# Optimization experiments

Measured on AMD Instinct MI355X. Metric: run time of the kernel, lower is better.

The kernel has to match this reference:

```python
import jax, jax.numpy as jnp
import numpy as np

EXP_CLAMP = 1.0e6
DENOM_EPS = 1e-10
LRELU_ALPHA = 0.01


def setup_inputs() -> dict:
    key = jax.random.key(0)
    k1, k2, k3, k4, k5, k6 = jax.random.split(key, 6)
    B, N, E, F = 4, 16384, 262144, 64
    h = jax.random.normal(k1, (B, N, F), dtype=jnp.float32)
    edge = jax.random.randint(k2, (B, E, 2), 0, N, dtype=jnp.int32)
    edge_num = jax.random.randint(k3, (B,), 1, E, dtype=jnp.int32)
    edge_weight = jax.random.uniform(k4, (B, E), dtype=jnp.float32)
    W = jax.random.normal(k5, (F, F), dtype=jnp.float32) * 0.15  # xavier-ish scale
    a = jax.random.normal(k6, (1, 2 * F), dtype=jnp.float32) * 0.12
    return {"h": h, "edge": edge, "edge_num": edge_num,
            "edge_weight": edge_weight, "W": W, "a": a}


def _seg_sum(src, idx, num_segments):
    # src: [E, ...], idx: [E] -> [num_segments, ...]
    return jax.ops.segment_sum(src, idx, num_segments=num_segments)


def reference(h, edge, edge_num, edge_weight, W, a):
    B, N, Fin = h.shape
    E = edge.shape[1]
    # linear transform: Wh = h @ W^T  -> [B, N, Fout]
    Wh = jnp.einsum('bnf,of->bno', h, W)
    ctr = edge[:, :, 0]  # [B, E]
    nbr = edge[:, :, 1]  # [B, E]
    Wh_c = jnp.take_along_axis(Wh, ctr[:, :, None], axis=1)  # [B, E, Fout]
    Wh_n = jnp.take_along_axis(Wh, nbr[:, :, None], axis=1)  # [B, E, Fout]
    a_input = jnp.concatenate([Wh_c, Wh_n], axis=-1) * edge_weight[:, :, None]
    # attention logits: leakyrelu(a_input @ a^T), squeeze to [B, E]
    att1 = jax.nn.leaky_relu(jnp.einsum('bek,k->be', a_input, a[0]), LRELU_ALPHA)
    # per-batch valid-edge mask (edges beyond edge_num zeroed, as in torch loop)
    mask = (jnp.arange(E, dtype=jnp.int32)[None, :] < edge_num[:, None])
    x_exp = jnp.clip(jnp.exp(att1), 0.0, EXP_CLAMP) * mask.astype(att1.dtype)
    # segment softmax denominator over center nodes
    denom = DENOM_EPS + jax.vmap(_seg_sum, in_axes=(0, 0, None))(x_exp, ctr, N)  # [B, N]
    att = x_exp / jnp.take_along_axis(denom, ctr, axis=1)  # [B, E]
    # weighted neighbor aggregation via scatter-add on center index
    att_Wh = Wh_n * att[:, :, None]  # masked edges already have att == 0
    h_prime = jax.vmap(_seg_sum, in_axes=(0, 0, None))(att_Wh, ctr, N)  # [B, N, Fout]
    return jax.nn.relu(h_prime)
```

## Files before the change

### kernel.cpp

```cpp
#include <hip/hip_runtime.h>

#define BB 4
#define NN 16384
#define EE 262144
#define FF 64
#define ROWS (BB * NN)
#define CAP 64
#define CHUNKS 64
#define CHUNK_E (EE / CHUNKS)
#define TILE_R 256
#define HALF_R (NN / 2)

typedef __bf16 bf16x8 __attribute__((ext_vector_type(8)));
typedef float  f32x4  __attribute__((ext_vector_type(4)));

__device__ __forceinline__ unsigned short f32_to_bf16(float f) {
    unsigned int u = __float_as_uint(f);
    u += 0x7FFFu + ((u >> 16) & 1u);
    return (unsigned short)(u >> 16);
}

__global__ __launch_bounds__(256) void mfma_kernel(
    const float* __restrict__ h, const float* __restrict__ W,
    const float* __restrict__ a,
    unsigned short* __restrict__ Wh,
    float* __restrict__ sc, float* __restrict__ sn)
{
    __shared__ float wc[FF], wn[FF];
    const int t = threadIdx.x;
    const int lane = t & 63;
    const int m = lane & 15;
    const int q = lane >> 4;

    if (t < 128) {
        const int f = t & 63;
        const float* av = a + (t >> 6) * FF;
        float s = 0.0f;
        #pragma unroll 8
        for (int o = 0; o < FF; ++o)
            s = fmaf(av[o], W[o * FF + f], s);
        (t < 64 ? wc : wn)[f] = s;
    }

    bf16x8 bfrag[4][2];
    #pragma unroll
    for (int nt = 0; nt < 4; ++nt) {
        const float* wr = W + (nt * 16 + m) * FF;
        #pragma unroll
        for (int kh = 0; kh < 2; ++kh) {
            const float4 v0 = *(const float4*)(wr + kh * 32 + q * 8);
            const float4 v1 = *(const float4*)(wr + kh * 32 + q * 8 + 4);
            bf16x8 b;
            b[0] = (__bf16)v0.x; b[1] = (__bf16)v0.y;
            b[2] = (__bf16)v0.z; b[3] = (__bf16)v0.w;
            b[4] = (__bf16)v1.x; b[5] = (__bf16)v1.y;
            b[6] = (__bf16)v1.z; b[7] = (__bf16)v1.w;
            bfrag[nt][kh] = b;
        }
    }

    __syncthreads();

    const int waveId = (blockIdx.x * 256 + t) >> 6;
    const int R0 = waveId * 16;
    const float* hr = h + (size_t)(R0 + m) * FF;
    bf16x8 af[2];
    float s1 = 0.0f, s2 = 0.0f;
    #pragma unroll
    for (int kh = 0; kh < 2; ++kh) {
        const float4 v0 = *(const float4*)(hr + kh * 32 + q * 8);
        const float4 v1 = *(const float4*)(hr + kh * 32 + q * 8 + 4);
        bf16x8 aa;
        aa[0] = (__bf16)v0.x; aa[1] = (__bf16)v0.y;
        aa[2] = (__bf16)v0.z; aa[3] = (__bf16)v0.w;
        aa[4] = (__bf16)v1.x; aa[5] = (__bf16)v1.y;
        aa[6] = (__bf16)v1.z; aa[7] = (__bf16)v1.w;
        af[kh] = aa;
        const int fb = kh * 32 + q * 8;
        const float4 c0 = *(const float4*)&wc[fb];
        const float4 c1 = *(const float4*)&wc[fb + 4];
        const float4 n0 = *(const float4*)&wn[fb];
        const float4 n1 = *(const float4*)&wn[fb + 4];
        s1 = fmaf(v0.x, c0.x, fmaf(v0.y, c0.y, fmaf(v0.z, c0.z, fmaf(v0.w, c0.w, s1))));
        s1 = fmaf(v1.x, c1.x, fmaf(v1.y, c1.y, fmaf(v1.z, c1.z, fmaf(v1.w, c1.w, s1))));
        s2 = fmaf(v0.x, n0.x, fmaf(v0.y, n0.y, fmaf(v0.z, n0.z, fmaf(v0.w, n0.w, s2))));
        s2 = fmaf(v1.x, n1.x, fmaf(v1.y, n1.y, fmaf(v1.z, n1.z, fmaf(v1.w, n1.w, s2))));
    }
    s1 += __shfl_xor(s1, 16); s2 += __shfl_xor(s2, 16);
    s1 += __shfl_xor(s1, 32); s2 += __shfl_xor(s2, 32);
    if (lane < 16) { sc[R0 + m] = s1; sn[R0 + m] = s2; }

    #pragma unroll
    for (int nt = 0; nt < 4; ++nt) {
        f32x4 acc = {0.f, 0.f, 0.f, 0.f};
        acc = __builtin_amdgcn_mfma_f32_16x16x32_bf16(af[0], bfrag[nt][0], acc, 0, 0, 0);
        acc = __builtin_amdgcn_mfma_f32_16x16x32_bf16(af[1], bfrag[nt][1], acc, 0, 0, 0);
        #pragma unroll
        for (int i = 0; i < 4; ++i)
            Wh[(size_t)(R0 + q * 4 + i) * FF + nt * 16 + m] = f32_to_bf16(acc[i]);
    }
}

__global__ __launch_bounds__(1024) void hist_kernel(
    const int* __restrict__ edge, const int* __restrict__ edge_num,
    unsigned short* __restrict__ histG)
{
    __shared__ unsigned int hist[HALF_R];
    const int g = blockIdx.x;
    const int half = g & 1;
    const int c = (g >> 1) & (CHUNKS - 1);
    const int b = g >> 7;
    const int t = threadIdx.x;
    const int en = edge_num[b];
    const int e0 = c * CHUNK_E;
    if (e0 >= en) return;

    for (int r = t; r < HALF_R; r += 1024) hist[r] = 0u;
    __syncthreads();

    const int2* ep = (const int2*)edge + (size_t)b * EE + e0;
    const int nAct = min(en - e0, CHUNK_E);
    for (int j = t; j < nAct; j += 1024) {
        const int2 e2 = ep[j];
        if ((e2.x >> 13) == half)
            atomicAdd(&hist[e2.x & (HALF_R - 1)], 1u);
    }
    __syncthreads();

    ushort2* out2 = (ushort2*)(histG + (size_t)(b * CHUNKS + c) * NN + half * HALF_R);
    for (int r2 = t; r2 < HALF_R / 2; r2 += 1024) {
        ushort2 v;
        v.x = (unsigned short)hist[2 * r2];
        v.y = (unsigned short)hist[2 * r2 + 1];
        out2[r2] = v;
    }
}

__global__ __launch_bounds__(256) void scan_kernel(
    const int* __restrict__ edge_num,
    unsigned short* __restrict__ histG, int* __restrict__ cnt)
{
    __shared__ unsigned short tile[CHUNKS][TILE_R];
    const int g = blockIdx.x;
    const int b = g >> 6, tl = g & 63;
    const int r0 = tl * TILE_R;
    const int t = threadIdx.x;
    const int en = edge_num[b];
    const int nact = min((en + CHUNK_E - 1) / CHUNK_E, CHUNKS);

    for (int c = 0; c < nact; ++c)
        tile[c][t] = histG[(size_t)(b * CHUNKS + c) * NN + r0 + t];
    __syncthreads();

    unsigned int acc = 0;
    for (int c = 0; c < nact; ++c) {
        const unsigned int v = tile[c][t];
        tile[c][t] = (unsigned short)(acc > 65535u ? 65535u : acc);
        acc += v;
    }
    cnt[b * NN + r0 + t] = (int)acc;

    for (int c = 0; c < nact; ++c)
        histG[(size_t)(b * CHUNKS + c) * NN + r0 + t] = tile[c][t];
}

__global__ __launch_bounds__(1024) void scatter_kernel(
    const int* __restrict__ edge, const int* __restrict__ edge_num,
    const unsigned short* __restrict__ baseG,
    const float* __restrict__ sc, const float* __restrict__ sn,
    const float* __restrict__ ew,
    unsigned int* __restrict__ payload)
{
    __shared__ unsigned int slotA[HALF_R];
    __shared__ float scL[HALF_R];
    const int g = blockIdx.x;
    const int half = g & 1;
    const int c = (g >> 1) & (CHUNKS - 1);
    const int b = g >> 7;
    const int t = threadIdx.x;
    const int en = edge_num[b];
    const int e0 = c * CHUNK_E;
    if (e0 >= en) return;

    const int rbase = half * HALF_R;
    const ushort2* b2 = (const ushort2*)(baseG + (size_t)(b * CHUNKS + c) * NN + rbase);
    for (int r2 = t; r2 < HALF_R / 2; r2 += 1024) {
        const ushort2 v = b2[r2];
        slotA[2 * r2]     = v.x;
        slotA[2 * r2 + 1] = v.y;
    }
    const float* scH = sc + b * NN + rbase;
    for (int r = t; r < HALF_R; r += 1024)
        scL[r] = scH[r];
    __syncthreads();

    const int2* ep = (const int2*)edge + (size_t)b * EE + e0;
    const int nAct = min(en - e0, CHUNK_E);
    const float* snB = sn + b * NN;
    const float* ewB = ew + (size_t)b * EE + e0;
    unsigned int* payB = payload + (size_t)b * NN * CAP;

    for (int j = t; j < nAct; j += 1024) {
        const int2 e2 = ep[j];
        if ((e2.x >> 13) != half) continue;
        const int rl = e2.x & (HALF_R - 1);
        const float wgt = ewB[j];
        const float s0 = wgt * (scL[rl] + snB[e2.y]);
        const float s1 = s0 > 0.0f ? s0 : 0.01f * s0;
        const float xe = fminf(__expf(s1), 1000000.0f);
        const unsigned int slot = atomicAdd(&slotA[rl], 1u);
        if (slot < CAP)
            payB[(size_t)e2.x * CAP + slot] =
                ((__float_as_uint(xe) + 0x2000u) & 0xFFFFC000u) | (unsigned int)e2.y;
    }
}

__global__ __launch_bounds__(256) void gather_kernel(
    const int* __restrict__ cnt, const unsigned int* __restrict__ payload,
    const uint2* __restrict__ Wh2,
    float* __restrict__ out)
{
    const int bi = blockIdx.x;
    const int xcd = bi & 7;
    const int batch = xcd >> 1;
    const int within = ((bi >> 3) << 1) | (xcd & 1);
    const int w = threadIdx.x >> 6;
    const int lane = threadIdx.x & 63;
    const int r = lane >> 4;
    const int f = lane & 15;
    const int gbase = lane & 48;
    const int rq = within * 4 + w;
    const int row = batch * NN + rq * 4 + r;

    const unsigned int* pl = payload + (size_t)row * CAP;
    const uint2* WhB = Wh2 + (size_t)batch * NN * 16;

    int deg = cnt[row];
    unsigned int raw = pl[f];
    if (deg > CAP) deg = CAP;

    int jmax = deg;
    jmax = max(jmax, __shfl_xor(jmax, 16));
    jmax = max(jmax, __shfl_xor(jmax, 32));

    float a0 = 0.f, a1 = 0.f, a2 = 0.f, a3 = 0.f, pdsum = 0.f;

    for (int base = 0; base < jmax; base += 16) {
        const unsigned int p = (base + f < deg) ? raw : 0u;
        pdsum += __uint_as_float(p & 0xFFFFC000u);

        unsigned int rawN = 0u;
        if (base + 16 < jmax) rawN = pl[base + 16 + f];

        const int lim = min(16, jmax - base);
        for (int j4 = 0; j4 < lim; j4 += 4) {
            const unsigned int pv0 = __shfl(p, gbase + j4 + 0);
            const unsigned int pv1 = __shfl(p, gbase + j4 + 1);
            const unsigned int pv2 = __shfl(p, gbase + j4 + 2);
            const unsigned int pv3 = __shfl(p, gbase + j4 + 3);
            const uint2 w0 = WhB[(size_t)(pv0 & 0x3FFFu) * 16 + f];
            const uint2 w1 = WhB[(size_t)(pv1 & 0x3FFFu) * 16 + f];
            const uint2 w2 = WhB[(size_t)(pv2 & 0x3FFFu) * 16 + f];
            const uint2 w3 = WhB[(size_t)(pv3 & 0x3FFFu) * 16 + f];
            const float xe0 = __uint_as_float(pv0 & 0xFFFFC000u);
            const float xe1 = __uint_as_float(pv1 & 0xFFFFC000u);
            const float xe2 = __uint_as_float(pv2 & 0xFFFFC000u);
            const float xe3 = __uint_as_float(pv3 & 0xFFFFC000u);
            a0 = fmaf(xe0, __uint_as_float(w0.x << 16),         a0);
            a1 = fmaf(xe0, __uint_as_float(w0.x & 0xFFFF0000u), a1);
            a2 = fmaf(xe0, __uint_as_float(w0.y << 16),         a2);
            a3 = fmaf(xe0, __uint_as_float(w0.y & 0xFFFF0000u), a3);
            a0 = fmaf(xe1, __uint_as_float(w1.x << 16),         a0);
            a1 = fmaf(xe1, __uint_as_float(w1.x & 0xFFFF0000u), a1);
            a2 = fmaf(xe1, __uint_as_float(w1.y << 16),         a2);
            a3 = fmaf(xe1, __uint_as_float(w1.y & 0xFFFF0000u), a3);
            a0 = fmaf(xe2, __uint_as_float(w2.x << 16),         a0);
            a1 = fmaf(xe2, __uint_as_float(w2.x & 0xFFFF0000u), a1);
            a2 = fmaf(xe2, __uint_as_float(w2.y << 16),         a2);
            a3 = fmaf(xe2, __uint_as_float(w2.y & 0xFFFF0000u), a3);
            a0 = fmaf(xe3, __uint_as_float(w3.x << 16),         a0);
            a1 = fmaf(xe3, __uint_as_float(w3.x & 0xFFFF0000u), a1);
            a2 = fmaf(xe3, __uint_as_float(w3.y << 16),         a2);
            a3 = fmaf(xe3, __uint_as_float(w3.y & 0xFFFF0000u), a3);
        }
        raw = rawN;
    }

    pdsum += __shfl_xor(pdsum, 1);
    pdsum += __shfl_xor(pdsum, 2);
    pdsum += __shfl_xor(pdsum, 4);
    pdsum += __shfl_xor(pdsum, 8);

    const float inv = 1.0f / (1e-10f + pdsum);
    float4 o;
    o.x = fmaxf(a0 * inv, 0.0f);
    o.y = fmaxf(a1 * inv, 0.0f);
    o.z = fmaxf(a2 * inv, 0.0f);
    o.w = fmaxf(a3 * inv, 0.0f);
    ((float4*)out)[(size_t)row * 16 + f] = o;
}

extern "C" void kernel_launch(void* const* d_in, const int* in_sizes, int n_in,
                              void* d_out, int out_size, void* d_ws, size_t ws_size,
                              hipStream_t stream)
{
    const float* h        = (const float*)d_in[0];
    const int*   edge     = (const int*)  d_in[1];
    const int*   edge_num = (const int*)  d_in[2];
    const float* ew       = (const float*)d_in[3];
    const float* W        = (const float*)d_in[4];
    const float* a        = (const float*)d_in[5];
    float* out = (float*)d_out;

    unsigned short* Wh = (unsigned short*)d_ws;
    float* sc        = (float*)(Wh + (size_t)BB * NN * FF);
    float* sn        = sc + ROWS;
    int*   cnt       = (int*)(sn + ROWS);
    unsigned int* payload = (unsigned int*)(cnt + ROWS);
    unsigned short* histG = (unsigned short*)(payload + (size_t)ROWS * CAP);

    mfma_kernel<<<1024, 256, 0, stream>>>(h, W, a, Wh, sc, sn);

    hist_kernel<<<BB * CHUNKS * 2, 1024, 0, stream>>>(edge, edge_num, histG);

    scan_kernel<<<BB * (NN / TILE_R), 256, 0, stream>>>(edge_num, histG, cnt);

    scatter_kernel<<<BB * CHUNKS * 2, 1024, 0, stream>>>(edge, edge_num, histG,
                                                         sc, sn, ew, payload);

    gather_kernel<<<4096, 256, 0, stream>>>(cnt, payload,
                                            (const uint2*)Wh, out);
}
```

Baseline: 130.3 us.

## Fuse the node-transform MFMA kernel with the edge histogram kernel

```diff
diff --git a/kernel.cpp b/kernel.cpp
--- a/kernel.cpp
+++ b/kernel.cpp
@@ -10,6 +10,7 @@
 #define CHUNK_E (EE / CHUNKS)
 #define TILE_R 256
 #define HALF_R (NN / 2)
+#define QUART_R (NN / 4)
 
 typedef __bf16 bf16x8 __attribute__((ext_vector_type(8)));
 typedef float  f32x4  __attribute__((ext_vector_type(4)));
@@ -20,17 +21,28 @@
     return (unsigned short)(u >> 16);
 }
 
-__global__ __launch_bounds__(256) void mfma_kernel(
+__global__ __launch_bounds__(256) void mfma_hist_kernel(
     const float* __restrict__ h, const float* __restrict__ W,
     const float* __restrict__ a,
+    const int* __restrict__ edge, const int* __restrict__ edge_num,
     unsigned short* __restrict__ Wh,
-    float* __restrict__ sc, float* __restrict__ sn)
+    float* __restrict__ sc, float* __restrict__ sn,
+    unsigned short* __restrict__ histG)
 {
     __shared__ float wc[FF], wn[FF];
+    __shared__ unsigned int hist[QUART_R];
     const int t = threadIdx.x;
     const int lane = t & 63;
     const int m = lane & 15;
     const int q = lane >> 4;
+
+    const int g = blockIdx.x;
+    const int b = g >> 8;
+    const int c = (g >> 2) & (CHUNKS - 1);
+    const int quarter = g & 3;
+    const int en = edge_num[b];
+    const int e0 = c * CHUNK_E;
+    const bool active = (e0 < en);
 
     if (t < 128) {
         const int f = t & 63;
@@ -41,6 +53,7 @@
             s = fmaf(av[o], W[o * FF + f], s);
         (t < 64 ? wc : wn)[f] = s;
     }
+    for (int r = t; r < QUART_R; r += 256) hist[r] = 0u;
 
     bf16x8 bfrag[4][2];
     #pragma unroll
@@ -50,89 +63,75 @@
         for (int kh = 0; kh < 2; ++kh) {
             const float4 v0 = *(const float4*)(wr + kh * 32 + q * 8);
             const float4 v1 = *(const float4*)(wr + kh * 32 + q * 8 + 4);
-            bf16x8 b;
-            b[0] = (__bf16)v0.x; b[1] = (__bf16)v0.y;
-            b[2] = (__bf16)v0.z; b[3] = (__bf16)v0.w;
-            b[4] = (__bf16)v1.x; b[5] = (__bf16)v1.y;
-            b[6] = (__bf16)v1.z; b[7] = (__bf16)v1.w;
-            bfrag[nt][kh] = b;
+            bf16x8 bb;
+            bb[0] = (__bf16)v0.x; bb[1] = (__bf16)v0.y;
+            bb[2] = (__bf16)v0.z; bb[3] = (__bf16)v0.w;
+            bb[4] = (__bf16)v1.x; bb[5] = (__bf16)v1.y;
+            bb[6] = (__bf16)v1.z; bb[7] = (__bf16)v1.w;
+            bfrag[nt][kh] = bb;
         }
     }
 
     __syncthreads();
 
-    const int waveId = (blockIdx.x * 256 + t) >> 6;
-    const int R0 = waveId * 16;
-    const float* hr = h + (size_t)(R0 + m) * FF;
-    bf16x8 af[2];
-    float s1 = 0.0f, s2 = 0.0f;
-    #pragma unroll
-    for (int kh = 0; kh < 2; ++kh) {
-        const float4 v0 = *(const float4*)(hr + kh * 32 + q * 8);
-        const float4 v1 = *(const float4*)(hr + kh * 32 + q * 8 + 4);
-        bf16x8 aa;
-        aa[0] = (__bf16)v0.x; aa[1] = (__bf16)v0.y;
-        aa[2] = (__bf16)v0.z; aa[3] = (__bf16)v0.w;
-        aa[4] = (__bf16)v1.x; aa[5] = (__bf16)v1.y;
-        aa[6] = (__bf16)v1.z; aa[7] = (__bf16)v1.w;
-        af[kh] = aa;
-        const int fb = kh * 32 + q * 8;
-        const float4 c0 = *(const float4*)&wc[fb];
-        const float4 c1 = *(const float4*)&wc[fb + 4];
-        const float4 n0 = *(const float4*)&wn[fb];
-        const float4 n1 = *(const float4*)&wn[fb + 4];
-        s1 = fmaf(v0.x, c0.x, fmaf(v0.y, c0.y, fmaf(v0.z, c0.z, fmaf(v0.w, c0.w, s1))));
-        s1 = fmaf(v1.x, c1.x, fmaf(v1.y, c1.y, fmaf(v1.z, c1.z, fmaf(v1.w, c1.w, s1))));
-        s2 = fmaf(v0.x, n0.x, fmaf(v0.y, n0.y, fmaf(v0.z, n0.z, fmaf(v0.w, n0.w, s2))));
-        s2 = fmaf(v1.x, n1.x, fmaf(v1.y, n1.y, fmaf(v1.z, n1.z, fmaf(v1.w, n1.w, s2))));
-    }
-    s1 += __shfl_xor(s1, 16); s2 += __shfl_xor(s2, 16);
-    s1 += __shfl_xor(s1, 32); s2 += __shfl_xor(s2, 32);
-    if (lane < 16) { sc[R0 + m] = s1; sn[R0 + m] = s2; }
-
-    #pragma unroll
-    for (int nt = 0; nt < 4; ++nt) {
-        f32x4 acc = {0.f, 0.f, 0.f, 0.f};
-        acc = __builtin_amdgcn_mfma_f32_16x16x32_bf16(af[0], bfrag[nt][0], acc, 0, 0, 0);
-        acc = __builtin_amdgcn_mfma_f32_16x16x32_bf16(af[1], bfrag[nt][1], acc, 0, 0, 0);
+    {
+        const int waveId = g * 4 + (t >> 6);
+        const int R0 = waveId * 16;
+        const float* hr = h + (size_t)(R0 + m) * FF;
+        bf16x8 af[2];
+        float s1 = 0.0f, s2 = 0.0f;
         #pragma unroll
-        for (int i = 0; i < 4; ++i)
-            Wh[(size_t)(R0 + q * 4 + i) * FF + nt * 16 + m] = f32_to_bf16(acc[i]);
-    }
-}
-
-__global__ __launch_bounds__(1024) void hist_kernel(
-    const int* __restrict__ edge, const int* __restrict__ edge_num,
-    unsigned short* __restrict__ histG)
-{
-    __shared__ unsigned int hist[HALF_R];
-    const int g = blockIdx.x;
-    const int half = g & 1;
-    const int c = (g >> 1) & (CHUNKS - 1);
-    const int b = g >> 7;
-    const int t = threadIdx.x;
-    const int en = edge_num[b];
-    const int e0 = c * CHUNK_E;
-    if (e0 >= en) return;
-
-    for (int r = t; r < HALF_R; r += 1024) hist[r] = 0u;
-    __syncthreads();
-
-    const int2* ep = (const int2*)edge + (size_t)b * EE + e0;
-    const int nAct = min(en - e0, CHUNK_E);
-    for (int j = t; j < nAct; j += 1024) {
-        const int2 e2 = ep[j];
-        if ((e2.x >> 13) == half)
-            atomicAdd(&hist[e2.x & (HALF_R - 1)], 1u);
-    }
-    __syncthreads();
-
-    ushort2* out2 = (ushort2*)(histG + (size_t)(b * CHUNKS + c) * NN + half * HALF_R);
-    for (int r2 = t; r2 < HALF_R / 2; r2 += 1024) {
-        ushort2 v;
-        v.x = (unsigned short)hist[2 * r2];
-        v.y = (unsigned short)hist[2 * r2 + 1];
-        out2[r2] = v;
+        for (int kh = 0; kh < 2; ++kh) {
+            const float4 v0 = *(const float4*)(hr + kh * 32 + q * 8);
+            const float4 v1 = *(const float4*)(hr + kh * 32 + q * 8 + 4);
+            bf16x8 aa;
+            aa[0] = (__bf16)v0.x; aa[1] = (__bf16)v0.y;
+            aa[2] = (__bf16)v0.z; aa[3] = (__bf16)v0.w;
+            aa[4] = (__bf16)v1.x; aa[5] = (__bf16)v1.y;
+            aa[6] = (__bf16)v1.z; aa[7] = (__bf16)v1.w;
+            af[kh] = aa;
+            const int fb = kh * 32 + q * 8;
+            const float4 c0 = *(const float4*)&wc[fb];
+            const float4 c1 = *(const float4*)&wc[fb + 4];
+            const float4 n0 = *(const float4*)&wn[fb];
+            const float4 n1 = *(const float4*)&wn[fb + 4];
+            s1 = fmaf(v0.x, c0.x, fmaf(v0.y, c0.y, fmaf(v0.z, c0.z, fmaf(v0.w, c0.w, s1))));
+            s1 = fmaf(v1.x, c1.x, fmaf(v1.y, c1.y, fmaf(v1.z, c1.z, fmaf(v1.w, c1.w, s1))));
+            s2 = fmaf(v0.x, n0.x, fmaf(v0.y, n0.y, fmaf(v0.z, n0.z, fmaf(v0.w, n0.w, s2))));
+            s2 = fmaf(v1.x, n1.x, fmaf(v1.y, n1.y, fmaf(v1.z, n1.z, fmaf(v1.w, n1.w, s2))));
+        }
+        s1 += __shfl_xor(s1, 16); s2 += __shfl_xor(s2, 16);
+        s1 += __shfl_xor(s1, 32); s2 += __shfl_xor(s2, 32);
+        if (lane < 16) { sc[R0 + m] = s1; sn[R0 + m] = s2; }
+
+        #pragma unroll
+        for (int nt = 0; nt < 4; ++nt) {
+            f32x4 acc = {0.f, 0.f, 0.f, 0.f};
+            acc = __builtin_amdgcn_mfma_f32_16x16x32_bf16(af[0], bfrag[nt][0], acc, 0, 0, 0);
+            acc = __builtin_amdgcn_mfma_f32_16x16x32_bf16(af[1], bfrag[nt][1], acc, 0, 0, 0);
+            #pragma unroll
+            for (int i = 0; i < 4; ++i)
+                Wh[(size_t)(R0 + q * 4 + i) * FF + nt * 16 + m] = f32_to_bf16(acc[i]);
+        }
+    }
+
+    if (active) {
+        const int2* ep = (const int2*)edge + (size_t)b * EE + e0;
+        const int nAct = min(en - e0, CHUNK_E);
+        for (int j = t; j < nAct; j += 256) {
+            const int2 e2 = ep[j];
+            if ((e2.x >> 12) == quarter)
+                atomicAdd(&hist[e2.x & (QUART_R - 1)], 1u);
+        }
+        __syncthreads();
+
+        ushort2* out2 = (ushort2*)(histG + (size_t)(b * CHUNKS + c) * NN + quarter * QUART_R);
+        for (int r2 = t; r2 < QUART_R / 2; r2 += 256) {
+            ushort2 v;
+            v.x = (unsigned short)hist[2 * r2];
+            v.y = (unsigned short)hist[2 * r2 + 1];
+            out2[r2] = v;
+        }
     }
 }
 
@@ -319,9 +318,8 @@
     unsigned int* payload = (unsigned int*)(cnt + ROWS);
     unsigned short* histG = (unsigned short*)(payload + (size_t)ROWS * CAP);
 
-    mfma_kernel<<<1024, 256, 0, stream>>>(h, W, a, Wh, sc, sn);
-
-    hist_kernel<<<BB * CHUNKS * 2, 1024, 0, stream>>>(edge, edge_num, histG);
+    mfma_hist_kernel<<<1024, 256, 0, stream>>>(h, W, a, edge, edge_num,
+                                               Wh, sc, sn, histG);
 
     scan_kernel<<<BB * (NN / TILE_R), 256, 0, stream>>>(edge_num, histG, cnt);
 
```

Result: slower. 136.4 us (+4.6%).
